# Kernel optimization log

Measured on AMD Instinct MI355X. Metric: run time of the kernel, lower is better.

## Reference

```python
import jax, jax.numpy as jnp
import numpy as np

EMBED_DIM = 1024
NUM_HEADS = 16
NUM_GROUPS = 4
HEAD_DIM = EMBED_DIM // NUM_HEADS
REPEAT = NUM_HEADS // NUM_GROUPS
MAX_TIME = 128
MAX_FREQ = 8


def build_relative_index(q_len, k_len, freq_size=MAX_FREQ, max_time=MAX_TIME, max_freq=MAX_FREQ):
    # static (numpy) construction; shapes are compile-time constants under jit
    q_time = q_len // max_freq
    k_time = k_len // max_freq
    qt = np.arange(q_time) + (k_time - q_time)
    q_coords = np.stack(np.meshgrid(qt, np.arange(freq_size), indexing='ij')).reshape(2, -1)
    k_coords = np.stack(np.meshgrid(np.arange(k_time), np.arange(freq_size), indexing='ij')).reshape(2, -1)
    rel = q_coords[:, :, None] - k_coords[:, None, :]  # [2, Nq, Nk]
    rel_t = np.clip(rel[0], -max_time + 1, max_time - 1) + max_time - 1
    rel_f = np.clip(rel[1], -max_freq + 1, max_freq - 1) + max_freq - 1
    return jnp.asarray(rel_t, jnp.int32), jnp.asarray(rel_f, jnp.int32)


def setup_inputs() -> dict:
    key = jax.random.key(0)
    ks = jax.random.split(key, 11)
    B, N, D, Nc = 2, 512, EMBED_DIM, 1536
    s = 0.02
    return {
        'q': jax.random.normal(ks[0], (B, N, D), jnp.float32),
        'k': jax.random.normal(ks[1], (B, N, D), jnp.float32),
        'v': jax.random.normal(ks[2], (B, N, D), jnp.float32),
        'attn_cache_k': jax.random.normal(ks[3], (B * NUM_HEADS, HEAD_DIM, Nc), jnp.float32),
        'attn_cache_v': jax.random.normal(ks[4], (B * NUM_HEADS, Nc, HEAD_DIM), jnp.float32),
        'Wq': jax.random.normal(ks[5], (D, D), jnp.float32) * s,
        'Wk': jax.random.normal(ks[6], (D, HEAD_DIM * NUM_GROUPS), jnp.float32) * s,
        'Wv': jax.random.normal(ks[7], (D, HEAD_DIM * NUM_GROUPS), jnp.float32) * s,
        'Wo': jax.random.normal(ks[8], (D, D), jnp.float32) * s,
        'emb_t': jax.random.normal(ks[9], (2 * MAX_TIME - 1, HEAD_DIM), jnp.float32) * s,
        'emb_f': jax.random.normal(ks[10], (2 * MAX_FREQ - 1, HEAD_DIM), jnp.float32) * s,
    }


def reference(q, k, v, attn_cache_k, attn_cache_v, Wq, Wk, Wv, Wo, emb_t, emb_f):
    B, N, D = q.shape
    H, G, hd, r = NUM_HEADS, NUM_GROUPS, HEAD_DIM, REPEAT
    # projections (no bias); head layout matches torch view: [B, N, H, hd] -> [B*H, N, hd]
    qp = (q @ Wq).reshape(B, N, H, hd).transpose(0, 2, 1, 3).reshape(B * H, N, hd)
    kp = (k @ Wk).reshape(B, N, G, hd).transpose(0, 2, 3, 1).reshape(B * G, hd, N)  # transposed K
    vp = (v @ Wv).reshape(B, N, G, hd).transpose(0, 2, 1, 3).reshape(B * G, N, hd)
    # GQA: repeat_interleave kv heads to query heads
    kp = jnp.repeat(kp, r, axis=0)
    vp = jnp.repeat(vp, r, axis=0)
    # streaming cache concat + slide
    k_full = jnp.concatenate([attn_cache_k, kp], axis=-1)            # [B*H, hd, Nk]
    new_cache_k = k_full[:, :, -attn_cache_k.shape[-1]:]
    v_full = jnp.concatenate([attn_cache_v, vp], axis=1)             # [B*H, Nk, hd]
    new_cache_v = v_full[:, -attn_cache_v.shape[1]:, :]
    Nk = k_full.shape[-1]
    qs = qp * (hd ** -0.5)
    scores = jnp.einsum('bid,bdj->bij', qs, k_full)                  # [B*H, N, Nk]
    rel_t, rel_f = build_relative_index(N, Nk)
    rel_emb = emb_t[rel_t] + emb_f[rel_f]                            # [N, Nk, hd]
    bias = jnp.einsum('bid,ijd->bij', qs, rel_emb)
    attn = jax.nn.softmax(scores + bias, axis=-1)
    ao = jnp.einsum('bij,bjd->bid', attn, v_full)                    # [B*H, N, hd]
    ao = ao.reshape(B, H, N, hd).transpose(2, 0, 1, 3).reshape(N, B, D)
    out = (ao @ Wo).transpose(1, 0, 2)                               # [B, N, D]
    return out, new_cache_k, new_cache_v
```

## Files before the change

### kernel.cpp

```cpp
#include <hip/hip_runtime.h>
#include <math.h>

typedef _Float16 half_t;
typedef _Float16 half8  __attribute__((ext_vector_type(8)));
typedef float    floatx4 __attribute__((ext_vector_type(4)));

static __device__ __forceinline__ floatx4 mfma16(half8 a, half8 b, floatx4 c) {
    return __builtin_amdgcn_mfma_f32_16x16x32_f16(a, b, c, 0, 0, 0);
}

__global__ __launch_bounds__(256) void prep(const float* __restrict__ cache_k,
                                            const float* __restrict__ cache_v,
                                            const float* __restrict__ Wq,
                                            const float* __restrict__ Wk,
                                            const float* __restrict__ Wv,
                                            const float* __restrict__ Wo,
                                            const float* __restrict__ emb_t,
                                            const float* __restrict__ emb_f,
                                            half_t* __restrict__ Kc,
                                            half_t* __restrict__ VcT,
                                            float* __restrict__ out_k,
                                            float* __restrict__ out_v,
                                            half_t* __restrict__ WqT,
                                            half_t* __restrict__ WkvT,
                                            half_t* __restrict__ WoT,
                                            half_t* __restrict__ embc)
{
    const int tid = threadIdx.x;
    const int z = blockIdx.z;
    __shared__ float t[64][65];
    if (z == 0) {
        const int bh = blockIdx.y, j0 = blockIdx.x * 64;
        for (int idx = tid; idx < 4096; idx += 256) {
            int d = idx >> 6, jj = idx & 63;
            float v = cache_k[((size_t)bh * 64 + d) * 1536 + j0 + jj];
            t[d][jj] = v;
            int js = j0 + jj;
            if (js >= 512) out_k[((size_t)bh * 64 + d) * 1536 + js - 512] = v;
        }
        __syncthreads();
        for (int idx = tid; idx < 4096; idx += 256) {
            int jj = idx >> 6, d = idx & 63;
            Kc[((size_t)bh * 1536 + j0 + jj) * 64 + d] = (half_t)t[d][jj];
        }
    } else if (z == 1) {
        const int bh = blockIdx.y, j0 = blockIdx.x * 64;
        for (int idx = tid; idx < 4096; idx += 256) {
            int jj = idx >> 6, d = idx & 63;
            float v = cache_v[((size_t)bh * 1536 + j0 + jj) * 64 + d];
            t[jj][d] = v;
            if (j0 + jj >= 512) out_v[((size_t)bh * 1536 + j0 + jj - 512) * 64 + d] = v;
        }
        __syncthreads();
        for (int idx = tid; idx < 4096; idx += 256) {
            int d = idx >> 6, jj = idx & 63;
            VcT[((size_t)bh * 64 + d) * 1536 + j0 + jj] = (half_t)t[jj][d];
        }
    } else {
        const int id = blockIdx.y * 24 + blockIdx.x;
        const float* src; half_t* dst; int Ncols, n0, k0;
        if (id < 256)      { src = Wq; dst = WqT; Ncols = 1024; n0 = (id & 15) * 64; k0 = (id >> 4) * 64; }
        else if (id < 320) { int q2 = id - 256; src = Wk; dst = WkvT; Ncols = 256; n0 = (q2 & 3) * 64; k0 = (q2 >> 2) * 64; }
        else if (id < 384) { int q2 = id - 320; src = Wv; dst = WkvT + 256 * 1024; Ncols = 256; n0 = (q2 & 3) * 64; k0 = (q2 >> 2) * 64; }
        else if (id < 640) { int q2 = id - 384; src = Wo; dst = WoT; Ncols = 1024; n0 = (q2 & 15) * 64; k0 = (q2 >> 4) * 64; }
        else if (id < 720) {
            int idx = (id - 640) * 256 + tid;
            int row = idx >> 6, col = idx & 63;
            float val = 0.f;
            if (row < 255) val = emb_t[row * 64 + col];
            else if (row >= 256 && row < 271) val = emb_f[(row - 256) * 64 + col];
            embc[idx] = (half_t)val;
            return;
        } else return;
        for (int idx = tid; idx < 4096; idx += 256) {
            int r = idx >> 6, cc = idx & 63;
            t[r][cc] = src[(size_t)(k0 + r) * Ncols + n0 + cc];
        }
        __syncthreads();
        for (int idx = tid; idx < 4096; idx += 256) {
            int r = idx >> 6, cc = idx & 63;
            dst[(size_t)(n0 + r) * 1024 + k0 + cc] = (half_t)t[cc][r];
        }
    }
}

__global__ __launch_bounds__(256) void proj(int phase,
                                            const float* __restrict__ qin,
                                            const float* __restrict__ kin,
                                            const float* __restrict__ vin,
                                            const half_t* __restrict__ AO,
                                            const half_t* __restrict__ WqT,
                                            const half_t* __restrict__ WkvT,
                                            const half_t* __restrict__ WoT,
                                            half_t* __restrict__ qs_h,
                                            half_t* __restrict__ kp_h,
                                            half_t* __restrict__ vpT,
                                            float* __restrict__ out,
                                            float* __restrict__ out_k,
                                            float* __restrict__ out_v)
{
    __shared__ __align__(16) half_t As[2][64 * 72];
    __shared__ __align__(16) half_t Bs[2][64 * 72];
    const int id = blockIdx.x;
    int task, m0, n0;
    const float* Af = nullptr; const half_t* Ah = nullptr; const half_t* Bt;
    if (phase == 1)      { task = 2; m0 = (id >> 4) * 64; n0 = (id & 15) * 64; Ah = AO; Bt = WoT; }
    else if (id < 256)   { task = 0; m0 = (id >> 4) * 64; n0 = (id & 15) * 64; Af = qin; Bt = WqT; }
    else { task = 1; int t = id - 256; m0 = (t >> 3) * 64; n0 = (t & 7) * 64;
           Af = (n0 < 256) ? kin : vin; Bt = WkvT; }

    const int tid = threadIdx.x, w = tid >> 6, l = tid & 63;
    const int quad = l >> 4, lr = l & 15, wm = w >> 1, wn = w & 1;
    const int arow = tid >> 2, acol = (tid & 3) * 16;

    {
        if (Af) {
            float4 f0 = *(const float4*)&Af[(size_t)(m0 + arow) * 1024 + acol];
            float4 f1 = *(const float4*)&Af[(size_t)(m0 + arow) * 1024 + acol + 4];
            float4 f2 = *(const float4*)&Af[(size_t)(m0 + arow) * 1024 + acol + 8];
            float4 f3 = *(const float4*)&Af[(size_t)(m0 + arow) * 1024 + acol + 12];
            half8 h0, h1;
            h0[0]=(half_t)f0.x; h0[1]=(half_t)f0.y; h0[2]=(half_t)f0.z; h0[3]=(half_t)f0.w;
            h0[4]=(half_t)f1.x; h0[5]=(half_t)f1.y; h0[6]=(half_t)f1.z; h0[7]=(half_t)f1.w;
            h1[0]=(half_t)f2.x; h1[1]=(half_t)f2.y; h1[2]=(half_t)f2.z; h1[3]=(half_t)f2.w;
            h1[4]=(half_t)f3.x; h1[5]=(half_t)f3.y; h1[6]=(half_t)f3.z; h1[7]=(half_t)f3.w;
            *(half8*)&As[0][arow * 72 + acol] = h0;
            *(half8*)&As[0][arow * 72 + acol + 8] = h1;
        } else {
            *(half8*)&As[0][arow * 72 + acol]     = *(const half8*)&Ah[(size_t)(m0 + arow) * 1024 + acol];
            *(half8*)&As[0][arow * 72 + acol + 8] = *(const half8*)&Ah[(size_t)(m0 + arow) * 1024 + acol + 8];
        }
        *(half8*)&Bs[0][arow * 72 + acol]     = *(const half8*)&Bt[(size_t)(n0 + arow) * 1024 + acol];
        *(half8*)&Bs[0][arow * 72 + acol + 8] = *(const half8*)&Bt[(size_t)(n0 + arow) * 1024 + acol + 8];
    }
    __syncthreads();

    floatx4 zero = {0.f, 0.f, 0.f, 0.f};
    floatx4 acc[2][2];
    acc[0][0] = zero; acc[0][1] = zero; acc[1][0] = zero; acc[1][1] = zero;

    float4 pf0, pf1, pf2, pf3; half8 ph0, ph1, pb0, pb1;
    for (int it = 0; it < 16; ++it) {
        if (it < 15) {
            int kk = (it + 1) * 64;
            if (Af) {
                pf0 = *(const float4*)&Af[(size_t)(m0 + arow) * 1024 + kk + acol];
                pf1 = *(const float4*)&Af[(size_t)(m0 + arow) * 1024 + kk + acol + 4];
                pf2 = *(const float4*)&Af[(size_t)(m0 + arow) * 1024 + kk + acol + 8];
                pf3 = *(const float4*)&Af[(size_t)(m0 + arow) * 1024 + kk + acol + 12];
            } else {
                ph0 = *(const half8*)&Ah[(size_t)(m0 + arow) * 1024 + kk + acol];
                ph1 = *(const half8*)&Ah[(size_t)(m0 + arow) * 1024 + kk + acol + 8];
            }
            pb0 = *(const half8*)&Bt[(size_t)(n0 + arow) * 1024 + kk + acol];
            pb1 = *(const half8*)&Bt[(size_t)(n0 + arow) * 1024 + kk + acol + 8];
        }
        const half_t* Ab = &As[it & 1][0];
        const half_t* Bb = &Bs[it & 1][0];
        #pragma unroll
        for (int ks = 0; ks < 2; ++ks) {
            half8 a0 = *(const half8*)&Ab[(wm * 32 + lr) * 72 + ks * 32 + quad * 8];
            half8 a1 = *(const half8*)&Ab[(wm * 32 + 16 + lr) * 72 + ks * 32 + quad * 8];
            half8 b0 = *(const half8*)&Bb[(wn * 32 + lr) * 72 + ks * 32 + quad * 8];
            half8 b1 = *(const half8*)&Bb[(wn * 32 + 16 + lr) * 72 + ks * 32 + quad * 8];
            acc[0][0] = mfma16(a0, b0, acc[0][0]);
            acc[0][1] = mfma16(a0, b1, acc[0][1]);
            acc[1][0] = mfma16(a1, b0, acc[1][0]);
            acc[1][1] = mfma16(a1, b1, acc[1][1]);
        }
        __syncthreads();
        if (it < 15) {
            int buf = (it + 1) & 1;
            if (Af) {
                half8 h0, h1;
                h0[0]=(half_t)pf0.x; h0[1]=(half_t)pf0.y; h0[2]=(half_t)pf0.z; h0[3]=(half_t)pf0.w;
                h0[4]=(half_t)pf1.x; h0[5]=(half_t)pf1.y; h0[6]=(half_t)pf1.z; h0[7]=(half_t)pf1.w;
                h1[0]=(half_t)pf2.x; h1[1]=(half_t)pf2.y; h1[2]=(half_t)pf2.z; h1[3]=(half_t)pf2.w;
                h1[4]=(half_t)pf3.x; h1[5]=(half_t)pf3.y; h1[6]=(half_t)pf3.z; h1[7]=(half_t)pf3.w;
                *(half8*)&As[buf][arow * 72 + acol] = h0;
                *(half8*)&As[buf][arow * 72 + acol + 8] = h1;
            } else {
                *(half8*)&As[buf][arow * 72 + acol] = ph0;
                *(half8*)&As[buf][arow * 72 + acol + 8] = ph1;
            }
            *(half8*)&Bs[buf][arow * 72 + acol] = pb0;
            *(half8*)&Bs[buf][arow * 72 + acol + 8] = pb1;
            __syncthreads();
        }
    }

    if (task == 0) {
        #pragma unroll
        for (int mi = 0; mi < 2; mi++)
            #pragma unroll
            for (int ni = 0; ni < 2; ni++)
                #pragma unroll
                for (int r = 0; r < 4; r++) {
                    int m = m0 + wm * 32 + mi * 16 + quad * 4 + r;
                    int n = n0 + wn * 32 + ni * 16 + lr;
                    qs_h[(size_t)m * 1024 + n] = (half_t)(acc[mi][ni][r] * 0.125f);
                }
    } else if (task == 2) {
        #pragma unroll
        for (int mi = 0; mi < 2; mi++)
            #pragma unroll
            for (int ni = 0; ni < 2; ni++)
                #pragma unroll
                for (int r = 0; r < 4; r++) {
                    int m = m0 + wm * 32 + mi * 16 + quad * 4 + r;
                    int n = n0 + wn * 32 + ni * 16 + lr;
                    out[(size_t)m * 1024 + n] = acc[mi][ni][r];
                }
    } else {
        __syncthreads();
        float* Ct = (float*)&As[0][0];
        #pragma unroll
        for (int mi = 0; mi < 2; mi++)
            #pragma unroll
            for (int ni = 0; ni < 2; ni++)
                #pragma unroll
                for (int r = 0; r < 4; r++)
                    Ct[(wn * 32 + ni * 16 + lr) * 68 + wm * 32 + mi * 16 + quad * 4 + r] = acc[mi][ni][r];
        __syncthreads();
        const int b = m0 >> 9, jm0 = m0 & 511;
        if (n0 < 256) {
            int gg = n0 >> 6;
            {
                int d = tid >> 2, jc = (tid & 3) * 16;
                float4 vv[4];
                #pragma unroll
                for (int u = 0; u < 4; u++) vv[u] = *(float4*)&Ct[d * 68 + jc + u * 4];
                #pragma unroll
                for (int t = 0; t < 4; t++)
                    #pragma unroll
                    for (int u = 0; u < 4; u++)
                        *(float4*)&out_k[((size_t)((b * 16 + gg * 4 + t) * 64 + d)) * 1536 + 1024 + jm0 + jc + u * 4] = vv[u];
            }
            {
                int j = tid >> 2, dc = (tid & 3) * 16;
                half8 o0, o1;
                #pragma unroll
                for (int u = 0; u < 8; u++) o0[u] = (half_t)Ct[(dc + u) * 68 + j];
                #pragma unroll
                for (int u = 0; u < 8; u++) o1[u] = (half_t)Ct[(dc + 8 + u) * 68 + j];
                *(half8*)&kp_h[((size_t)(b * 512 + jm0 + j)) * 256 + n0 + dc] = o0;
                *(half8*)&kp_h[((size_t)(b * 512 + jm0 + j)) * 256 + n0 + dc + 8] = o1;
            }
        } else {
            int gg = (n0 - 256) >> 6;
            {
                int j = tid >> 2, dc = (tid & 3) * 16;
                float4 vv[4];
                #pragma unroll
                for (int u = 0; u < 4; u++) {
                    float4 x;
                    x.x = Ct[(dc + u * 4 + 0) * 68 + j];
                    x.y = Ct[(dc + u * 4 + 1) * 68 + j];
                    x.z = Ct[(dc + u * 4 + 2) * 68 + j];
                    x.w = Ct[(dc + u * 4 + 3) * 68 + j];
                    vv[u] = x;
                }
                #pragma unroll
                for (int t = 0; t < 4; t++)
                    #pragma unroll
                    for (int u = 0; u < 4; u++)
                        *(float4*)&out_v[(((size_t)(b * 16 + gg * 4 + t) * 1536) + 1024 + jm0 + j) * 64 + dc + u * 4] = vv[u];
            }
            {
                int d = tid >> 2, jc = (tid & 3) * 16;
                half8 o0, o1;
                #pragma unroll
                for (int u = 0; u < 8; u++) o0[u] = (half_t)Ct[d * 68 + jc + u];
                #pragma unroll
                for (int u = 0; u < 8; u++) o1[u] = (half_t)Ct[d * 68 + jc + 8 + u];
                *(half8*)&vpT[((size_t)((b * 4 + gg) * 64 + d)) * 512 + jm0 + jc] = o0;
                *(half8*)&vpT[((size_t)((b * 4 + gg) * 64 + d)) * 512 + jm0 + jc + 8] = o1;
            }
        }
    }
}

__global__ __launch_bounds__(256) void flash(const half_t* __restrict__ qs_h,
                                             const half_t* __restrict__ Kc,
                                             const half_t* __restrict__ kp_h,
                                             const half_t* __restrict__ VcT,
                                             const half_t* __restrict__ vpT,
                                             const half_t* __restrict__ embc,
                                             half_t* __restrict__ AO)
{
    __shared__ __align__(16) half_t Qs[64 * 72];
    __shared__ __align__(16) half_t Ks[128 * 72];
    __shared__ __align__(16) half_t Vs[64 * 136];
    __shared__ __align__(16) half_t Ps[64 * 136];
    __shared__ half_t bt[64 * 322];
    const int bh = blockIdx.y, b = bh >> 4, h = bh & 15, g = h >> 2;
    const int i0 = blockIdx.x * 64;
    const int tid = threadIdx.x, w = tid >> 6, l = tid & 63;
    const int quad = l >> 4, lr = l & 15;

    {
        int row = tid >> 2, c = (tid & 3) * 16;
        const half_t* src = &qs_h[((size_t)(b * 512 + i0 + row)) * 1024 + h * 64 + c];
        *(half8*)&Qs[row * 72 + c]     = *(const half8*)src;
        *(half8*)&Qs[row * 72 + c + 8] = *(const half8*)(src + 8);
    }

    const int krow = tid >> 1, kcb = (tid & 1) * 32;
    const int vd = tid >> 2, vcb = (tid & 3) * 32;
    half8 kr[4], vr[4];
    {
        const half_t* ksrc = &Kc[((size_t)bh * 1536 + krow) * 64 + kcb];
        const half_t* vsrc = &VcT[((size_t)bh * 64 + vd) * 1536 + vcb];
        #pragma unroll
        for (int u = 0; u < 4; u++) kr[u] = *(const half8*)(ksrc + u * 8);
        #pragma unroll
        for (int u = 0; u < 4; u++) vr[u] = *(const half8*)(vsrc + u * 8);
    }
    __syncthreads();

    half8 af0 = *(const half8*)&Qs[(w * 16 + lr) * 72 + quad * 8];
    half8 af1 = *(const half8*)&Qs[(w * 16 + lr) * 72 + 32 + quad * 8];

    floatx4 zero = {0.f, 0.f, 0.f, 0.f};
    #pragma unroll 4
    for (int nf = 0; nf < 20; ++nf) {
        floatx4 acc = zero;
        half8 b0 = *(const half8*)&embc[(size_t)(nf * 16 + lr) * 64 + quad * 8];
        half8 b1 = *(const half8*)&embc[(size_t)(nf * 16 + lr) * 64 + 32 + quad * 8];
        acc = mfma16(af0, b0, acc);
        acc = mfma16(af1, b1, acc);
        #pragma unroll
        for (int r = 0; r < 4; r++)
            bt[(w * 16 + quad * 4 + r) * 322 + nf * 16 + lr] = (half_t)acc[r];
    }

    #pragma unroll
    for (int u = 0; u < 4; u++) *(half8*)&Ks[krow * 72 + kcb + u * 8] = kr[u];
    #pragma unroll
    for (int u = 0; u < 4; u++) *(half8*)&Vs[vd * 136 + vcb + u * 8] = vr[u];
    __syncthreads();

    float bfv[4];
    int qtr[4];
    #pragma unroll
    for (int r = 0; r < 4; r++) {
        int f = ((quad & 1) * 4 + r) - (lr & 7) + 7;
        bfv[r] = (float)bt[(w * 16 + quad * 4 + r) * 322 + 256 + f];
        qtr[r] = (i0 + w * 16 + quad * 4 + r) >> 3;
    }

    floatx4 accO[4];
    #pragma unroll
    for (int ni = 0; ni < 4; ni++) accO[ni] = zero;
    float mrun[4] = {-1e30f, -1e30f, -1e30f, -1e30f};
    float lrun[4] = {0.f, 0.f, 0.f, 0.f};

    for (int jt = 0; jt < 16; ++jt) {
        if (jt < 15) {
            const int j1 = (jt + 1) * 128;
            const half_t* ksrc = (j1 < 1536)
                ? &Kc[((size_t)bh * 1536 + j1 + krow) * 64 + kcb]
                : &kp_h[((size_t)(b * 512 + j1 - 1536 + krow)) * 256 + g * 64 + kcb];
            const half_t* vsrc = (j1 < 1536)
                ? &VcT[((size_t)bh * 64 + vd) * 1536 + j1 + vcb]
                : &vpT[((size_t)(b * 4 + g) * 64 + vd) * 512 + (j1 - 1536) + vcb];
            #pragma unroll
            for (int u = 0; u < 4; u++) kr[u] = *(const half8*)(ksrc + u * 8);
            #pragma unroll
            for (int u = 0; u < 4; u++) vr[u] = *(const half8*)(vsrc + u * 8);
        }

        floatx4 s[8];
        #pragma unroll
        for (int nj = 0; nj < 8; nj++) {
            half8 b0 = *(const half8*)&Ks[(nj * 16 + lr) * 72 + quad * 8];
            half8 b1 = *(const half8*)&Ks[(nj * 16 + lr) * 72 + 32 + quad * 8];
            s[nj] = mfma16(af0, b0, zero);
            s[nj] = mfma16(af1, b1, s[nj]);
        }
        const int jtt = jt * 16;
        #pragma unroll
        for (int nj = 0; nj < 8; nj++)
            #pragma unroll
            for (int r = 0; r < 4; r++) {
                int t = 319 + qtr[r] - jtt - (nj * 2 + (lr >> 3));
                t = min(t, 254);
                s[nj][r] += (float)bt[(w * 16 + quad * 4 + r) * 322 + t] + bfv[r];
            }
        float tmax[4];
        #pragma unroll
        for (int r = 0; r < 4; r++) {
            float tm = s[0][r];
            #pragma unroll
            for (int nj = 1; nj < 8; nj++) tm = fmaxf(tm, s[nj][r]);
            tm = fmaxf(tm, __shfl_xor(tm, 1));
            tm = fmaxf(tm, __shfl_xor(tm, 2));
            tm = fmaxf(tm, __shfl_xor(tm, 4));
            tm = fmaxf(tm, __shfl_xor(tm, 8));
            tmax[r] = tm;
        }
        float alpha[4];
        #pragma unroll
        for (int r = 0; r < 4; r++) {
            float mn = fmaxf(mrun[r], tmax[r]);
            alpha[r] = __expf(mrun[r] - mn);
            mrun[r] = mn;
        }
        float psum[4] = {0.f, 0.f, 0.f, 0.f};
        #pragma unroll
        for (int nj = 0; nj < 8; nj++)
            #pragma unroll
            for (int r = 0; r < 4; r++) {
                float p = __expf(s[nj][r] - mrun[r]);
                s[nj][r] = p;
                psum[r] += p;
            }
        #pragma unroll
        for (int r = 0; r < 4; r++) {
            float ps = psum[r];
            ps += __shfl_xor(ps, 1);
            ps += __shfl_xor(ps, 2);
            ps += __shfl_xor(ps, 4);
            ps += __shfl_xor(ps, 8);
            lrun[r] = lrun[r] * alpha[r] + ps;
        }
        #pragma unroll
        for (int ni = 0; ni < 4; ni++)
            #pragma unroll
            for (int r = 0; r < 4; r++) accO[ni][r] *= alpha[r];
        #pragma unroll
        for (int nj = 0; nj < 8; nj++)
            #pragma unroll
            for (int r = 0; r < 4; r++)
                Ps[(w * 16 + quad * 4 + r) * 136 + nj * 16 + lr] = (half_t)s[nj][r];
        #pragma unroll
        for (int ks = 0; ks < 4; ks++) {
            half8 pa = *(const half8*)&Ps[(w * 16 + lr) * 136 + ks * 32 + quad * 8];
            #pragma unroll
            for (int ni = 0; ni < 4; ni++) {
                half8 vb = *(const half8*)&Vs[(ni * 16 + lr) * 136 + ks * 32 + quad * 8];
                accO[ni] = mfma16(pa, vb, accO[ni]);
            }
        }
        __syncthreads();
        if (jt < 15) {
            #pragma unroll
            for (int u = 0; u < 4; u++) *(half8*)&Ks[krow * 72 + kcb + u * 8] = kr[u];
            #pragma unroll
            for (int u = 0; u < 4; u++) *(half8*)&Vs[vd * 136 + vcb + u * 8] = vr[u];
            __syncthreads();
        }
    }

    float inv[4];
    #pragma unroll
    for (int r = 0; r < 4; r++) inv[r] = 1.0f / lrun[r];
    #pragma unroll
    for (int ni = 0; ni < 4; ni++)
        #pragma unroll
        for (int r = 0; r < 4; r++) {
            int i = i0 + w * 16 + quad * 4 + r;
            AO[((size_t)(b * 512 + i)) * 1024 + h * 64 + ni * 16 + lr] =
                (half_t)(accO[ni][r] * inv[r]);
        }
}

extern "C" void kernel_launch(void* const* d_in, const int* in_sizes, int n_in,
                              void* d_out, int out_size, void* d_ws, size_t ws_size,
                              hipStream_t stream)
{
    const float* q       = (const float*)d_in[0];
    const float* k       = (const float*)d_in[1];
    const float* v       = (const float*)d_in[2];
    const float* cache_k = (const float*)d_in[3];
    const float* cache_v = (const float*)d_in[4];
    const float* Wq      = (const float*)d_in[5];
    const float* Wk      = (const float*)d_in[6];
    const float* Wv      = (const float*)d_in[7];
    const float* Wo      = (const float*)d_in[8];
    const float* emb_t   = (const float*)d_in[9];
    const float* emb_f   = (const float*)d_in[10];

    float* out   = (float*)d_out;
    float* out_k = out + 1048576;
    float* out_v = out_k + 3145728;

    half_t* ws = (half_t*)d_ws;
    half_t* qs_h = ws;
    half_t* kp_h = ws + 1048576;
    half_t* vpT  = ws + 1310720;
    half_t* Kc   = ws + 1572864;
    half_t* VcT  = ws + 4718592;
    half_t* WqT  = ws + 7864320;
    half_t* WkvT = ws + 8912896;
    half_t* WoT  = ws + 9437184;
    half_t* embc = ws + 10485760;
    half_t* AO   = ws + 10506240;

    prep<<<dim3(24, 32, 3), 256, 0, stream>>>(cache_k, cache_v, Wq, Wk, Wv, Wo,
                                              emb_t, emb_f, Kc, VcT, out_k, out_v,
                                              WqT, WkvT, WoT, embc);
    proj<<<dim3(384), 256, 0, stream>>>(0, q, k, v, nullptr, WqT, WkvT, WoT,
                                        qs_h, kp_h, vpT, out, out_k, out_v);
    flash<<<dim3(8, 32), 256, 0, stream>>>(qs_h, Kc, kp_h, VcT, vpT, embc, AO);
    proj<<<dim3(256), 256, 0, stream>>>(1, q, k, v, AO, WqT, WkvT, WoT,
                                        qs_h, kp_h, vpT, out, out_k, out_v);
}
```

Baseline: 198.0 us.

## Split-K projections, split-KV flash attention, vectorized prep, exp2 softmax

The projection GEMM now uses 512 threads, with two halves of the block each reducing half of K and merging through shared memory. Flash attention also uses 512 threads and splits each key tile between two wave groups, merging their partial softmax states at the end. The log2e factor is folded into the query scale so the softmax can use exp2f. The prep transposes now use float4 loads and half8 stores. The goal is more parallelism per block and less memory-instruction overhead, at the cost of extra shared memory, a reduction step and higher register pressure.

```diff
diff --git a/kernel.cpp b/kernel.cpp
--- a/kernel.cpp
+++ b/kernel.cpp
@@ -4,6 +4,8 @@
 typedef _Float16 half_t;
 typedef _Float16 half8  __attribute__((ext_vector_type(8)));
 typedef float    floatx4 __attribute__((ext_vector_type(4)));
+
+#define LOG2E 1.44269504088896f
 
 static __device__ __forceinline__ floatx4 mfma16(half8 a, half8 b, floatx4 c) {
     return __builtin_amdgcn_mfma_f32_16x16x32_f16(a, b, c, 0, 0, 0);
@@ -31,30 +33,45 @@
     __shared__ float t[64][65];
     if (z == 0) {
         const int bh = blockIdx.y, j0 = blockIdx.x * 64;
-        for (int idx = tid; idx < 4096; idx += 256) {
-            int d = idx >> 6, jj = idx & 63;
-            float v = cache_k[((size_t)bh * 64 + d) * 1536 + j0 + jj];
-            t[d][jj] = v;
-            int js = j0 + jj;
-            if (js >= 512) out_k[((size_t)bh * 64 + d) * 1536 + js - 512] = v;
+        const bool shift = (j0 >= 512);
+        #pragma unroll
+        for (int i2 = 0; i2 < 4; i2++) {
+            int idx = i2 * 256 + tid;
+            int d = idx >> 4, j4 = (idx & 15) * 4;
+            float4 vv = *(const float4*)&cache_k[((size_t)bh * 64 + d) * 1536 + j0 + j4];
+            *(float4*)&t[d][j4] = vv;
+            if (shift) *(float4*)&out_k[((size_t)bh * 64 + d) * 1536 + j0 - 512 + j4] = vv;
         }
         __syncthreads();
-        for (int idx = tid; idx < 4096; idx += 256) {
-            int jj = idx >> 6, d = idx & 63;
-            Kc[((size_t)bh * 1536 + j0 + jj) * 64 + d] = (half_t)t[d][jj];
+        #pragma unroll
+        for (int i2 = 0; i2 < 2; i2++) {
+            int idx = i2 * 256 + tid;
+            int j = idx >> 3, db = (idx & 7) * 8;
+            half8 o;
+            #pragma unroll
+            for (int u = 0; u < 8; u++) o[u] = (half_t)t[db + u][j];
+            *(half8*)&Kc[((size_t)bh * 1536 + j0 + j) * 64 + db] = o;
         }
     } else if (z == 1) {
         const int bh = blockIdx.y, j0 = blockIdx.x * 64;
-        for (int idx = tid; idx < 4096; idx += 256) {
-            int jj = idx >> 6, d = idx & 63;
-            float v = cache_v[((size_t)bh * 1536 + j0 + jj) * 64 + d];
-            t[jj][d] = v;
-            if (j0 + jj >= 512) out_v[((size_t)bh * 1536 + j0 + jj - 512) * 64 + d] = v;
+        const bool shift = (j0 >= 512);
+        #pragma unroll
+        for (int i2 = 0; i2 < 4; i2++) {
+            int idx = i2 * 256 + tid;
+            int j = idx >> 4, d4 = (idx & 15) * 4;
+            float4 vv = *(const float4*)&cache_v[((size_t)bh * 1536 + j0 + j) * 64 + d4];
+            *(float4*)&t[j][d4] = vv;
+            if (shift) *(float4*)&out_v[((size_t)bh * 1536 + j0 + j - 512) * 64 + d4] = vv;
         }
         __syncthreads();
-        for (int idx = tid; idx < 4096; idx += 256) {
-            int d = idx >> 6, jj = idx & 63;
-            VcT[((size_t)bh * 64 + d) * 1536 + j0 + jj] = (half_t)t[jj][d];
+        #pragma unroll
+        for (int i2 = 0; i2 < 2; i2++) {
+            int idx = i2 * 256 + tid;
+            int d = idx >> 3, jb = (idx & 7) * 8;
+            half8 o;
+            #pragma unroll
+            for (int u = 0; u < 8; u++) o[u] = (half_t)t[jb + u][d];
+            *(half8*)&VcT[((size_t)bh * 64 + d) * 1536 + j0 + jb] = o;
         }
     } else {
         const int id = blockIdx.y * 24 + blockIdx.x;
@@ -72,19 +89,26 @@
             embc[idx] = (half_t)val;
             return;
         } else return;
-        for (int idx = tid; idx < 4096; idx += 256) {
-            int r = idx >> 6, cc = idx & 63;
-            t[r][cc] = src[(size_t)(k0 + r) * Ncols + n0 + cc];
+        #pragma unroll
+        for (int i2 = 0; i2 < 4; i2++) {
+            int idx = i2 * 256 + tid;
+            int r = idx >> 4, c4 = (idx & 15) * 4;
+            *(float4*)&t[r][c4] = *(const float4*)&src[(size_t)(k0 + r) * Ncols + n0 + c4];
         }
         __syncthreads();
-        for (int idx = tid; idx < 4096; idx += 256) {
-            int r = idx >> 6, cc = idx & 63;
-            dst[(size_t)(n0 + r) * 1024 + k0 + cc] = (half_t)t[cc][r];
+        #pragma unroll
+        for (int i2 = 0; i2 < 2; i2++) {
+            int idx = i2 * 256 + tid;
+            int n = idx >> 3, kb = (idx & 7) * 8;
+            half8 o;
+            #pragma unroll
+            for (int u = 0; u < 8; u++) o[u] = (half_t)t[kb + u][n];
+            *(half8*)&dst[(size_t)(n0 + n) * 1024 + k0 + kb] = o;
         }
     }
 }
 
-__global__ __launch_bounds__(256) void proj(int phase,
+__global__ __launch_bounds__(512) void proj(int phase,
                                             const float* __restrict__ qin,
                                             const float* __restrict__ kin,
                                             const float* __restrict__ vin,
@@ -99,8 +123,8 @@
                                             float* __restrict__ out_k,
                                             float* __restrict__ out_v)
 {
-    __shared__ __align__(16) half_t As[2][64 * 72];
-    __shared__ __align__(16) half_t Bs[2][64 * 72];
+    __shared__ __align__(16) half_t As[2][2][64 * 72];
+    __shared__ __align__(16) half_t Bs[2][2][64 * 72];
     const int id = blockIdx.x;
     int task, m0, n0;
     const float* Af = nullptr; const half_t* Ah = nullptr; const half_t* Bt;
@@ -109,29 +133,33 @@
     else { task = 1; int t = id - 256; m0 = (t >> 3) * 64; n0 = (t & 7) * 64;
            Af = (n0 < 256) ? kin : vin; Bt = WkvT; }
 
-    const int tid = threadIdx.x, w = tid >> 6, l = tid & 63;
-    const int quad = l >> 4, lr = l & 15, wm = w >> 1, wn = w & 1;
-    const int arow = tid >> 2, acol = (tid & 3) * 16;
+    const int tid = threadIdx.x;
+    const int kh = tid >> 8, t8 = tid & 255;
+    const int w4 = (tid >> 6) & 3, l = tid & 63;
+    const int quad = l >> 4, lr = l & 15, wm = w4 >> 1, wn = w4 & 1;
+    const int arow = t8 >> 2, acol = (t8 & 3) * 16;
+    const int kbase = kh * 512;
 
     {
+        int kk = kbase;
         if (Af) {
-            float4 f0 = *(const float4*)&Af[(size_t)(m0 + arow) * 1024 + acol];
-            float4 f1 = *(const float4*)&Af[(size_t)(m0 + arow) * 1024 + acol + 4];
-            float4 f2 = *(const float4*)&Af[(size_t)(m0 + arow) * 1024 + acol + 8];
-            float4 f3 = *(const float4*)&Af[(size_t)(m0 + arow) * 1024 + acol + 12];
+            float4 f0 = *(const float4*)&Af[(size_t)(m0 + arow) * 1024 + kk + acol];
+            float4 f1 = *(const float4*)&Af[(size_t)(m0 + arow) * 1024 + kk + acol + 4];
+            float4 f2 = *(const float4*)&Af[(size_t)(m0 + arow) * 1024 + kk + acol + 8];
+            float4 f3 = *(const float4*)&Af[(size_t)(m0 + arow) * 1024 + kk + acol + 12];
             half8 h0, h1;
             h0[0]=(half_t)f0.x; h0[1]=(half_t)f0.y; h0[2]=(half_t)f0.z; h0[3]=(half_t)f0.w;
             h0[4]=(half_t)f1.x; h0[5]=(half_t)f1.y; h0[6]=(half_t)f1.z; h0[7]=(half_t)f1.w;
             h1[0]=(half_t)f2.x; h1[1]=(half_t)f2.y; h1[2]=(half_t)f2.z; h1[3]=(half_t)f2.w;
             h1[4]=(half_t)f3.x; h1[5]=(half_t)f3.y; h1[6]=(half_t)f3.z; h1[7]=(half_t)f3.w;
-            *(half8*)&As[0][arow * 72 + acol] = h0;
-            *(half8*)&As[0][arow * 72 + acol + 8] = h1;
+            *(half8*)&As[kh][0][arow * 72 + acol] = h0;
+            *(half8*)&As[kh][0][arow * 72 + acol + 8] = h1;
         } else {
-            *(half8*)&As[0][arow * 72 + acol]     = *(const half8*)&Ah[(size_t)(m0 + arow) * 1024 + acol];
-            *(half8*)&As[0][arow * 72 + acol + 8] = *(const half8*)&Ah[(size_t)(m0 + arow) * 1024 + acol + 8];
-        }
-        *(half8*)&Bs[0][arow * 72 + acol]     = *(const half8*)&Bt[(size_t)(n0 + arow) * 1024 + acol];
-        *(half8*)&Bs[0][arow * 72 + acol + 8] = *(const half8*)&Bt[(size_t)(n0 + arow) * 1024 + acol + 8];
+            *(half8*)&As[kh][0][arow * 72 + acol]     = *(const half8*)&Ah[(size_t)(m0 + arow) * 1024 + kk + acol];
+            *(half8*)&As[kh][0][arow * 72 + acol + 8] = *(const half8*)&Ah[(size_t)(m0 + arow) * 1024 + kk + acol + 8];
+        }
+        *(half8*)&Bs[kh][0][arow * 72 + acol]     = *(const half8*)&Bt[(size_t)(n0 + arow) * 1024 + kk + acol];
+        *(half8*)&Bs[kh][0][arow * 72 + acol + 8] = *(const half8*)&Bt[(size_t)(n0 + arow) * 1024 + kk + acol + 8];
     }
     __syncthreads();
 
@@ -140,9 +168,9 @@
     acc[0][0] = zero; acc[0][1] = zero; acc[1][0] = zero; acc[1][1] = zero;
 
     float4 pf0, pf1, pf2, pf3; half8 ph0, ph1, pb0, pb1;
-    for (int it = 0; it < 16; ++it) {
-        if (it < 15) {
-            int kk = (it + 1) * 64;
+    for (int it = 0; it < 8; ++it) {
+        if (it < 7) {
+            int kk = kbase + (it + 1) * 64;
             if (Af) {
                 pf0 = *(const float4*)&Af[(size_t)(m0 + arow) * 1024 + kk + acol];
                 pf1 = *(const float4*)&Af[(size_t)(m0 + arow) * 1024 + kk + acol + 4];
@@ -155,8 +183,8 @@
             pb0 = *(const half8*)&Bt[(size_t)(n0 + arow) * 1024 + kk + acol];
             pb1 = *(const half8*)&Bt[(size_t)(n0 + arow) * 1024 + kk + acol + 8];
         }
-        const half_t* Ab = &As[it & 1][0];
-        const half_t* Bb = &Bs[it & 1][0];
+        const half_t* Ab = &As[kh][it & 1][0];
+        const half_t* Bb = &Bs[kh][it & 1][0];
         #pragma unroll
         for (int ks = 0; ks < 2; ++ks) {
             half8 a0 = *(const half8*)&Ab[(wm * 32 + lr) * 72 + ks * 32 + quad * 8];
@@ -169,7 +197,7 @@
             acc[1][1] = mfma16(a1, b1, acc[1][1]);
         }
         __syncthreads();
-        if (it < 15) {
+        if (it < 7) {
             int buf = (it + 1) & 1;
             if (Af) {
                 half8 h0, h1;
@@ -177,110 +205,138 @@
                 h0[4]=(half_t)pf1.x; h0[5]=(half_t)pf1.y; h0[6]=(half_t)pf1.z; h0[7]=(half_t)pf1.w;
                 h1[0]=(half_t)pf2.x; h1[1]=(half_t)pf2.y; h1[2]=(half_t)pf2.z; h1[3]=(half_t)pf2.w;
                 h1[4]=(half_t)pf3.x; h1[5]=(half_t)pf3.y; h1[6]=(half_t)pf3.z; h1[7]=(half_t)pf3.w;
-                *(half8*)&As[buf][arow * 72 + acol] = h0;
-                *(half8*)&As[buf][arow * 72 + acol + 8] = h1;
+                *(half8*)&As[kh][buf][arow * 72 + acol] = h0;
+                *(half8*)&As[kh][buf][arow * 72 + acol + 8] = h1;
             } else {
-                *(half8*)&As[buf][arow * 72 + acol] = ph0;
-                *(half8*)&As[buf][arow * 72 + acol + 8] = ph1;
-            }
-            *(half8*)&Bs[buf][arow * 72 + acol] = pb0;
-            *(half8*)&Bs[buf][arow * 72 + acol + 8] = pb1;
+                *(half8*)&As[kh][buf][arow * 72 + acol] = ph0;
+                *(half8*)&As[kh][buf][arow * 72 + acol + 8] = ph1;
+            }
+            *(half8*)&Bs[kh][buf][arow * 72 + acol] = pb0;
+            *(half8*)&Bs[kh][buf][arow * 72 + acol + 8] = pb1;
             __syncthreads();
         }
     }
 
-    if (task == 0) {
-        #pragma unroll
-        for (int mi = 0; mi < 2; mi++)
-            #pragma unroll
-            for (int ni = 0; ni < 2; ni++)
-                #pragma unroll
-                for (int r = 0; r < 4; r++) {
-                    int m = m0 + wm * 32 + mi * 16 + quad * 4 + r;
-                    int n = n0 + wn * 32 + ni * 16 + lr;
-                    qs_h[(size_t)m * 1024 + n] = (half_t)(acc[mi][ni][r] * 0.125f);
-                }
-    } else if (task == 2) {
-        #pragma unroll
-        for (int mi = 0; mi < 2; mi++)
-            #pragma unroll
-            for (int ni = 0; ni < 2; ni++)
-                #pragma unroll
-                for (int r = 0; r < 4; r++) {
-                    int m = m0 + wm * 32 + mi * 16 + quad * 4 + r;
-                    int n = n0 + wn * 32 + ni * 16 + lr;
-                    out[(size_t)m * 1024 + n] = acc[mi][ni][r];
-                }
-    } else {
-        __syncthreads();
-        float* Ct = (float*)&As[0][0];
+    float* M = (float*)&Bs[0][0][0];
+    if (kh == 1) {
         #pragma unroll
         for (int mi = 0; mi < 2; mi++)
             #pragma unroll
             for (int ni = 0; ni < 2; ni++)
                 #pragma unroll
                 for (int r = 0; r < 4; r++)
-                    Ct[(wn * 32 + ni * 16 + lr) * 68 + wm * 32 + mi * 16 + quad * 4 + r] = acc[mi][ni][r];
+                    M[(wm * 32 + mi * 16 + quad * 4 + r) * 66 + wn * 32 + ni * 16 + lr] = acc[mi][ni][r];
+    }
+    __syncthreads();
+    if (kh == 0) {
+        #pragma unroll
+        for (int mi = 0; mi < 2; mi++)
+            #pragma unroll
+            for (int ni = 0; ni < 2; ni++)
+                #pragma unroll
+                for (int r = 0; r < 4; r++)
+                    acc[mi][ni][r] += M[(wm * 32 + mi * 16 + quad * 4 + r) * 66 + wn * 32 + ni * 16 + lr];
+    }
+
+    if (task == 0) {
+        if (kh == 0) {
+            #pragma unroll
+            for (int mi = 0; mi < 2; mi++)
+                #pragma unroll
+                for (int ni = 0; ni < 2; ni++)
+                    #pragma unroll
+                    for (int r = 0; r < 4; r++) {
+                        int m = m0 + wm * 32 + mi * 16 + quad * 4 + r;
+                        int n = n0 + wn * 32 + ni * 16 + lr;
+                        qs_h[(size_t)m * 1024 + n] = (half_t)(acc[mi][ni][r] * (0.125f * LOG2E));
+                    }
+        }
+    } else if (task == 2) {
+        if (kh == 0) {
+            #pragma unroll
+            for (int mi = 0; mi < 2; mi++)
+                #pragma unroll
+                for (int ni = 0; ni < 2; ni++)
+                    #pragma unroll
+                    for (int r = 0; r < 4; r++) {
+                        int m = m0 + wm * 32 + mi * 16 + quad * 4 + r;
+                        int n = n0 + wn * 32 + ni * 16 + lr;
+                        out[(size_t)m * 1024 + n] = acc[mi][ni][r];
+                    }
+        }
+    } else {
+        float* Ct = (float*)&As[0][0][0];
+        if (kh == 0) {
+            #pragma unroll
+            for (int mi = 0; mi < 2; mi++)
+                #pragma unroll
+                for (int ni = 0; ni < 2; ni++)
+                    #pragma unroll
+                    for (int r = 0; r < 4; r++)
+                        Ct[(wn * 32 + ni * 16 + lr) * 68 + wm * 32 + mi * 16 + quad * 4 + r] = acc[mi][ni][r];
+        }
         __syncthreads();
-        const int b = m0 >> 9, jm0 = m0 & 511;
-        if (n0 < 256) {
-            int gg = n0 >> 6;
-            {
-                int d = tid >> 2, jc = (tid & 3) * 16;
-                float4 vv[4];
-                #pragma unroll
-                for (int u = 0; u < 4; u++) vv[u] = *(float4*)&Ct[d * 68 + jc + u * 4];
-                #pragma unroll
-                for (int t = 0; t < 4; t++)
-                    #pragma unroll
-                    for (int u = 0; u < 4; u++)
-                        *(float4*)&out_k[((size_t)((b * 16 + gg * 4 + t) * 64 + d)) * 1536 + 1024 + jm0 + jc + u * 4] = vv[u];
-            }
-            {
-                int j = tid >> 2, dc = (tid & 3) * 16;
-                half8 o0, o1;
-                #pragma unroll
-                for (int u = 0; u < 8; u++) o0[u] = (half_t)Ct[(dc + u) * 68 + j];
-                #pragma unroll
-                for (int u = 0; u < 8; u++) o1[u] = (half_t)Ct[(dc + 8 + u) * 68 + j];
-                *(half8*)&kp_h[((size_t)(b * 512 + jm0 + j)) * 256 + n0 + dc] = o0;
-                *(half8*)&kp_h[((size_t)(b * 512 + jm0 + j)) * 256 + n0 + dc + 8] = o1;
-            }
-        } else {
-            int gg = (n0 - 256) >> 6;
-            {
-                int j = tid >> 2, dc = (tid & 3) * 16;
-                float4 vv[4];
-                #pragma unroll
-                for (int u = 0; u < 4; u++) {
-                    float4 x;
-                    x.x = Ct[(dc + u * 4 + 0) * 68 + j];
-                    x.y = Ct[(dc + u * 4 + 1) * 68 + j];
-                    x.z = Ct[(dc + u * 4 + 2) * 68 + j];
-                    x.w = Ct[(dc + u * 4 + 3) * 68 + j];
-                    vv[u] = x;
+        if (kh == 0) {
+            const int b = m0 >> 9, jm0 = m0 & 511;
+            if (n0 < 256) {
+                int gg = n0 >> 6;
+                {
+                    int d = t8 >> 2, jc = (t8 & 3) * 16;
+                    float4 vv[4];
+                    #pragma unroll
+                    for (int u = 0; u < 4; u++) vv[u] = *(float4*)&Ct[d * 68 + jc + u * 4];
+                    #pragma unroll
+                    for (int t = 0; t < 4; t++)
+                        #pragma unroll
+                        for (int u = 0; u < 4; u++)
+                            *(float4*)&out_k[((size_t)((b * 16 + gg * 4 + t) * 64 + d)) * 1536 + 1024 + jm0 + jc + u * 4] = vv[u];
                 }
-                #pragma unroll
-                for (int t = 0; t < 4; t++)
-                    #pragma unroll
-                    for (int u = 0; u < 4; u++)
-                        *(float4*)&out_v[(((size_t)(b * 16 + gg * 4 + t) * 1536) + 1024 + jm0 + j) * 64 + dc + u * 4] = vv[u];
-            }
-            {
-                int d = tid >> 2, jc = (tid & 3) * 16;
-                half8 o0, o1;
-                #pragma unroll
-                for (int u = 0; u < 8; u++) o0[u] = (half_t)Ct[d * 68 + jc + u];
-                #pragma unroll
-                for (int u = 0; u < 8; u++) o1[u] = (half_t)Ct[d * 68 + jc + 8 + u];
-                *(half8*)&vpT[((size_t)((b * 4 + gg) * 64 + d)) * 512 + jm0 + jc] = o0;
-                *(half8*)&vpT[((size_t)((b * 4 + gg) * 64 + d)) * 512 + jm0 + jc + 8] = o1;
+                {
+                    int j = t8 >> 2, dc = (t8 & 3) * 16;
+                    half8 o0, o1;
+                    #pragma unroll
+                    for (int u = 0; u < 8; u++) o0[u] = (half_t)Ct[(dc + u) * 68 + j];
+                    #pragma unroll
+                    for (int u = 0; u < 8; u++) o1[u] = (half_t)Ct[(dc + 8 + u) * 68 + j];
+                    *(half8*)&kp_h[((size_t)(b * 512 + jm0 + j)) * 256 + n0 + dc] = o0;
+                    *(half8*)&kp_h[((size_t)(b * 512 + jm0 + j)) * 256 + n0 + dc + 8] = o1;
+                }
+            } else {
+                int gg = (n0 - 256) >> 6;
+                {
+                    int j = t8 >> 2, dc = (t8 & 3) * 16;
+                    float4 vv[4];
+                    #pragma unroll
+                    for (int u = 0; u < 4; u++) {
+                        float4 x;
+                        x.x = Ct[(dc + u * 4 + 0) * 68 + j];
+                        x.y = Ct[(dc + u * 4 + 1) * 68 + j];
+                        x.z = Ct[(dc + u * 4 + 2) * 68 + j];
+                        x.w = Ct[(dc + u * 4 + 3) * 68 + j];
+                        vv[u] = x;
+                    }
+                    #pragma unroll
+                    for (int t = 0; t < 4; t++)
+                        #pragma unroll
+                        for (int u = 0; u < 4; u++)
+                            *(float4*)&out_v[(((size_t)(b * 16 + gg * 4 + t) * 1536) + 1024 + jm0 + j) * 64 + dc + u * 4] = vv[u];
+                }
+                {
+                    int d = t8 >> 2, jc = (t8 & 3) * 16;
+                    half8 o0, o1;
+                    #pragma unroll
+                    for (int u = 0; u < 8; u++) o0[u] = (half_t)Ct[d * 68 + jc + u];
+                    #pragma unroll
+                    for (int u = 0; u < 8; u++) o1[u] = (half_t)Ct[d * 68 + jc + 8 + u];
+                    *(half8*)&vpT[((size_t)((b * 4 + gg) * 64 + d)) * 512 + jm0 + jc] = o0;
+                    *(half8*)&vpT[((size_t)((b * 4 + gg) * 64 + d)) * 512 + jm0 + jc + 8] = o1;
+                }
             }
         }
     }
 }
 
-__global__ __launch_bounds__(256) void flash(const half_t* __restrict__ qs_h,
+__global__ __launch_bounds__(512) void flash(const half_t* __restrict__ qs_h,
                                              const half_t* __restrict__ Kc,
                                              const half_t* __restrict__ kp_h,
                                              const half_t* __restrict__ VcT,
@@ -292,38 +348,32 @@
     __shared__ __align__(16) half_t Ks[128 * 72];
     __shared__ __align__(16) half_t Vs[64 * 136];
     __shared__ __align__(16) half_t Ps[64 * 136];
-    __shared__ half_t bt[64 * 322];
-    const int bh = blockIdx.y, b = bh >> 4, h = bh & 15, g = h >> 2;
-    const int i0 = blockIdx.x * 64;
+    __shared__ half_t bt[64 * 210];
+    const int bh = blockIdx.x, b = bh >> 4, h = bh & 15, g = h >> 2;
+    const int i0 = blockIdx.y * 64;
     const int tid = threadIdx.x, w = tid >> 6, l = tid & 63;
     const int quad = l >> 4, lr = l & 15;
-
+    const int wq = w >> 1, jh = w & 1;
+
+    *(half8*)&Qs[(tid >> 3) * 72 + (tid & 7) * 8] =
+        *(const half8*)&qs_h[((size_t)(b * 512 + i0 + (tid >> 3))) * 1024 + h * 64 + (tid & 7) * 8];
+
+    const int krow = tid >> 2, kc = (tid & 3) * 16;
+    const int vd = tid >> 3, vc = (tid & 7) * 16;
+    half8 kr0, kr1, vr0, vr1;
     {
-        int row = tid >> 2, c = (tid & 3) * 16;
-        const half_t* src = &qs_h[((size_t)(b * 512 + i0 + row)) * 1024 + h * 64 + c];
-        *(half8*)&Qs[row * 72 + c]     = *(const half8*)src;
-        *(half8*)&Qs[row * 72 + c + 8] = *(const half8*)(src + 8);
-    }
-
-    const int krow = tid >> 1, kcb = (tid & 1) * 32;
-    const int vd = tid >> 2, vcb = (tid & 3) * 32;
-    half8 kr[4], vr[4];
-    {
-        const half_t* ksrc = &Kc[((size_t)bh * 1536 + krow) * 64 + kcb];
-        const half_t* vsrc = &VcT[((size_t)bh * 64 + vd) * 1536 + vcb];
-        #pragma unroll
-        for (int u = 0; u < 4; u++) kr[u] = *(const half8*)(ksrc + u * 8);
-        #pragma unroll
-        for (int u = 0; u < 4; u++) vr[u] = *(const half8*)(vsrc + u * 8);
+        const half_t* ksrc = &Kc[((size_t)bh * 1536 + krow) * 64 + kc];
+        const half_t* vsrc = &VcT[((size_t)bh * 64 + vd) * 1536 + vc];
+        kr0 = *(const half8*)ksrc; kr1 = *(const half8*)(ksrc + 8);
+        vr0 = *(const half8*)vsrc; vr1 = *(const half8*)(vsrc + 8);
     }
     __syncthreads();
 
-    half8 af0 = *(const half8*)&Qs[(w * 16 + lr) * 72 + quad * 8];
-    half8 af1 = *(const half8*)&Qs[(w * 16 + lr) * 72 + 32 + quad * 8];
+    half8 af0 = *(const half8*)&Qs[(wq * 16 + lr) * 72 + quad * 8];
+    half8 af1 = *(const half8*)&Qs[(wq * 16 + lr) * 72 + 32 + quad * 8];
 
     floatx4 zero = {0.f, 0.f, 0.f, 0.f};
-    #pragma unroll 4
-    for (int nf = 0; nf < 20; ++nf) {
+    for (int nf = 4 + jh * 6; nf < (jh ? 17 : 10); ++nf) {
         floatx4 acc = zero;
         half8 b0 = *(const half8*)&embc[(size_t)(nf * 16 + lr) * 64 + quad * 8];
         half8 b1 = *(const half8*)&embc[(size_t)(nf * 16 + lr) * 64 + 32 + quad * 8];
@@ -331,13 +381,13 @@
         acc = mfma16(af1, b1, acc);
         #pragma unroll
         for (int r = 0; r < 4; r++)
-            bt[(w * 16 + quad * 4 + r) * 322 + nf * 16 + lr] = (half_t)acc[r];
-    }
-
-    #pragma unroll
-    for (int u = 0; u < 4; u++) *(half8*)&Ks[krow * 72 + kcb + u * 8] = kr[u];
-    #pragma unroll
-    for (int u = 0; u < 4; u++) *(half8*)&Vs[vd * 136 + vcb + u * 8] = vr[u];
+            bt[(wq * 16 + quad * 4 + r) * 210 + nf * 16 + lr - 64] = (half_t)acc[r];
+    }
+
+    *(half8*)&Ks[krow * 72 + kc] = kr0;
+    *(half8*)&Ks[krow * 72 + kc + 8] = kr1;
+    *(half8*)&Vs[vd * 136 + vc] = vr0;
+    *(half8*)&Vs[vd * 136 + vc + 8] = vr1;
     __syncthreads();
 
     float bfv[4];
@@ -345,8 +395,8 @@
     #pragma unroll
     for (int r = 0; r < 4; r++) {
         int f = ((quad & 1) * 4 + r) - (lr & 7) + 7;
-        bfv[r] = (float)bt[(w * 16 + quad * 4 + r) * 322 + 256 + f];
-        qtr[r] = (i0 + w * 16 + quad * 4 + r) >> 3;
+        bfv[r] = (float)bt[(wq * 16 + quad * 4 + r) * 210 + 192 + f];
+        qtr[r] = (i0 + wq * 16 + quad * 4 + r) >> 3;
     }
 
     floatx4 accO[4];
@@ -359,59 +409,51 @@
         if (jt < 15) {
             const int j1 = (jt + 1) * 128;
             const half_t* ksrc = (j1 < 1536)
-                ? &Kc[((size_t)bh * 1536 + j1 + krow) * 64 + kcb]
-                : &kp_h[((size_t)(b * 512 + j1 - 1536 + krow)) * 256 + g * 64 + kcb];
+                ? &Kc[((size_t)bh * 1536 + j1 + krow) * 64 + kc]
+                : &kp_h[((size_t)(b * 512 + j1 - 1536 + krow)) * 256 + g * 64 + kc];
             const half_t* vsrc = (j1 < 1536)
-                ? &VcT[((size_t)bh * 64 + vd) * 1536 + j1 + vcb]
-                : &vpT[((size_t)(b * 4 + g) * 64 + vd) * 512 + (j1 - 1536) + vcb];
-            #pragma unroll
-            for (int u = 0; u < 4; u++) kr[u] = *(const half8*)(ksrc + u * 8);
-            #pragma unroll
-            for (int u = 0; u < 4; u++) vr[u] = *(const half8*)(vsrc + u * 8);
-        }
-
-        floatx4 s[8];
-        #pragma unroll
-        for (int nj = 0; nj < 8; nj++) {
-            half8 b0 = *(const half8*)&Ks[(nj * 16 + lr) * 72 + quad * 8];
-            half8 b1 = *(const half8*)&Ks[(nj * 16 + lr) * 72 + 32 + quad * 8];
+                ? &VcT[((size_t)bh * 64 + vd) * 1536 + j1 + vc]
+                : &vpT[((size_t)(b * 4 + g) * 64 + vd) * 512 + (j1 - 1536) + vc];
+            kr0 = *(const half8*)ksrc; kr1 = *(const half8*)(ksrc + 8);
+            vr0 = *(const half8*)vsrc; vr1 = *(const half8*)(vsrc + 8);
+        }
+
+        floatx4 s[4];
+        #pragma unroll
+        for (int nj = 0; nj < 4; nj++) {
+            int row = jh * 64 + nj * 16 + lr;
+            half8 b0 = *(const half8*)&Ks[row * 72 + quad * 8];
+            half8 b1 = *(const half8*)&Ks[row * 72 + 32 + quad * 8];
             s[nj] = mfma16(af0, b0, zero);
             s[nj] = mfma16(af1, b1, s[nj]);
         }
-        const int jtt = jt * 16;
-        #pragma unroll
-        for (int nj = 0; nj < 8; nj++)
+        const int ktb = jt * 16 + jh * 8 + (lr >> 3);
+        #pragma unroll
+        for (int nj = 0; nj < 4; nj++)
             #pragma unroll
             for (int r = 0; r < 4; r++) {
-                int t = 319 + qtr[r] - jtt - (nj * 2 + (lr >> 3));
-                t = min(t, 254);
-                s[nj][r] += (float)bt[(w * 16 + quad * 4 + r) * 322 + t] + bfv[r];
-            }
-        float tmax[4];
+                int toff = 255 + qtr[r] - (ktb + nj * 2);
+                toff = min(toff, 190);
+                s[nj][r] += (float)bt[(wq * 16 + quad * 4 + r) * 210 + toff] + bfv[r];
+            }
+        float alpha[4];
         #pragma unroll
         for (int r = 0; r < 4; r++) {
-            float tm = s[0][r];
-            #pragma unroll
-            for (int nj = 1; nj < 8; nj++) tm = fmaxf(tm, s[nj][r]);
+            float tm = fmaxf(fmaxf(s[0][r], s[1][r]), fmaxf(s[2][r], s[3][r]));
             tm = fmaxf(tm, __shfl_xor(tm, 1));
             tm = fmaxf(tm, __shfl_xor(tm, 2));
             tm = fmaxf(tm, __shfl_xor(tm, 4));
             tm = fmaxf(tm, __shfl_xor(tm, 8));
-            tmax[r] = tm;
-        }
-        float alpha[4];
-        #pragma unroll
-        for (int r = 0; r < 4; r++) {
-            float mn = fmaxf(mrun[r], tmax[r]);
-            alpha[r] = __expf(mrun[r] - mn);
+            float mn = fmaxf(mrun[r], tm);
+            alpha[r] = exp2f(mrun[r] - mn);
             mrun[r] = mn;
         }
         float psum[4] = {0.f, 0.f, 0.f, 0.f};
         #pragma unroll
-        for (int nj = 0; nj < 8; nj++)
+        for (int nj = 0; nj < 4; nj++)
             #pragma unroll
             for (int r = 0; r < 4; r++) {
-                float p = __expf(s[nj][r] - mrun[r]);
+                float p = exp2f(s[nj][r] - mrun[r]);
                 s[nj][r] = p;
                 psum[r] += p;
             }
@@ -429,40 +471,65 @@
             #pragma unroll
             for (int r = 0; r < 4; r++) accO[ni][r] *= alpha[r];
         #pragma unroll
-        for (int nj = 0; nj < 8; nj++)
+        for (int nj = 0; nj < 4; nj++)
             #pragma unroll
             for (int r = 0; r < 4; r++)
-                Ps[(w * 16 + quad * 4 + r) * 136 + nj * 16 + lr] = (half_t)s[nj][r];
-        #pragma unroll
-        for (int ks = 0; ks < 4; ks++) {
-            half8 pa = *(const half8*)&Ps[(w * 16 + lr) * 136 + ks * 32 + quad * 8];
+                Ps[(wq * 16 + quad * 4 + r) * 136 + jh * 64 + nj * 16 + lr] = (half_t)s[nj][r];
+        #pragma unroll
+        for (int ks = 0; ks < 2; ks++) {
+            half8 pa = *(const half8*)&Ps[(wq * 16 + lr) * 136 + jh * 64 + ks * 32 + quad * 8];
             #pragma unroll
             for (int ni = 0; ni < 4; ni++) {
-                half8 vb = *(const half8*)&Vs[(ni * 16 + lr) * 136 + ks * 32 + quad * 8];
+                half8 vb = *(const half8*)&Vs[(ni * 16 + lr) * 136 + jh * 64 + ks * 32 + quad * 8];
                 accO[ni] = mfma16(pa, vb, accO[ni]);
             }
         }
         __syncthreads();
         if (jt < 15) {
-            #pragma unroll
-            for (int u = 0; u < 4; u++) *(half8*)&Ks[krow * 72 + kcb + u * 8] = kr[u];
-            #pragma unroll
-            for (int u = 0; u < 4; u++) *(half8*)&Vs[vd * 136 + vcb + u * 8] = vr[u];
+            *(half8*)&Ks[krow * 72 + kc] = kr0;
+            *(half8*)&Ks[krow * 72 + kc + 8] = kr1;
+            *(half8*)&Vs[vd * 136 + vc] = vr0;
+            *(half8*)&Vs[vd * 136 + vc + 8] = vr1;
             __syncthreads();
         }
     }
 
-    float inv[4];
-    #pragma unroll
-    for (int r = 0; r < 4; r++) inv[r] = 1.0f / lrun[r];
-    #pragma unroll
-    for (int ni = 0; ni < 4; ni++)
+    float* MB = (float*)Ks;
+    float* ML = (float*)Vs;
+    if (jh == 1) {
         #pragma unroll
         for (int r = 0; r < 4; r++) {
-            int i = i0 + w * 16 + quad * 4 + r;
-            AO[((size_t)(b * 512 + i)) * 1024 + h * 64 + ni * 16 + lr] =
-                (half_t)(accO[ni][r] * inv[r]);
-        }
+            int row = wq * 16 + quad * 4 + r;
+            ML[row] = mrun[r];
+            ML[64 + row] = lrun[r];
+        }
+        #pragma unroll
+        for (int ni = 0; ni < 4; ni++)
+            #pragma unroll
+            for (int r = 0; r < 4; r++)
+                MB[(wq * 16 + quad * 4 + r) * 66 + ni * 16 + lr] = accO[ni][r];
+    }
+    __syncthreads();
+    if (jh == 0) {
+        float sc0[4], sc1[4];
+        #pragma unroll
+        for (int r = 0; r < 4; r++) {
+            int row = wq * 16 + quad * 4 + r;
+            float m1 = ML[row], l1 = ML[64 + row];
+            float m = fmaxf(mrun[r], m1);
+            float a0 = exp2f(mrun[r] - m), a1 = exp2f(m1 - m);
+            float inv = 1.0f / (lrun[r] * a0 + l1 * a1);
+            sc0[r] = a0 * inv; sc1[r] = a1 * inv;
+        }
+        #pragma unroll
+        for (int ni = 0; ni < 4; ni++)
+            #pragma unroll
+            for (int r = 0; r < 4; r++) {
+                int row = wq * 16 + quad * 4 + r;
+                float o = accO[ni][r] * sc0[r] + MB[row * 66 + ni * 16 + lr] * sc1[r];
+                AO[((size_t)(b * 512 + i0 + row)) * 1024 + h * 64 + ni * 16 + lr] = (half_t)o;
+            }
+    }
 }
 
 extern "C" void kernel_launch(void* const* d_in, const int* in_sizes, int n_in,
@@ -500,9 +567,9 @@
     prep<<<dim3(24, 32, 3), 256, 0, stream>>>(cache_k, cache_v, Wq, Wk, Wv, Wo,
                                               emb_t, emb_f, Kc, VcT, out_k, out_v,
                                               WqT, WkvT, WoT, embc);
-    proj<<<dim3(384), 256, 0, stream>>>(0, q, k, v, nullptr, WqT, WkvT, WoT,
+    proj<<<dim3(384), 512, 0, stream>>>(0, q, k, v, nullptr, WqT, WkvT, WoT,
                                         qs_h, kp_h, vpT, out, out_k, out_v);
-    flash<<<dim3(8, 32), 256, 0, stream>>>(qs_h, Kc, kp_h, VcT, vpT, embc, AO);
-    proj<<<dim3(256), 256, 0, stream>>>(1, q, k, v, AO, WqT, WkvT, WoT,
+    flash<<<dim3(32, 8), 512, 0, stream>>>(qs_h, Kc, kp_h, VcT, vpT, embc, AO);
+    proj<<<dim3(256), 512, 0, stream>>>(1, q, k, v, AO, WqT, WkvT, WoT,
                                         qs_h, kp_h, vpT, out, out_k, out_v);
 }
```

Result: faster. 181.4 us (-8.3%).
